# Performance work log

Hardware: AMD Instinct MI355X
Metric: run time of the kernel (lower is better)

The kernel has to match this reference:

```python
import jax, jax.numpy as jnp
import numpy as np

N_NODES = 50000
N_EDGES = 600000
IN_C, HID, OUT_C, HEADS = 128, 64, 16, 4


def setup_inputs() -> dict:
    key = jax.random.key(0)
    ks = jax.random.split(key, 12)
    s = 1.0 / np.sqrt(HID)
    return {
        "x": jax.random.normal(ks[0], (N_NODES, IN_C), dtype=jnp.float32),
        "edge_index": jax.random.randint(ks[1], (2, N_EDGES), 0, N_NODES, dtype=jnp.int64),
        "W_lin": jax.random.normal(ks[2], (IN_C, HID), dtype=jnp.float32) / np.sqrt(IN_C),
        "b_lin": jnp.zeros((HID,), dtype=jnp.float32),
        "Wq": jax.random.normal(ks[3], (HID, HID), dtype=jnp.float32) * s,
        "bq": jnp.zeros((HID,), dtype=jnp.float32),
        "Wk": jax.random.normal(ks[4], (HID, HID), dtype=jnp.float32) * s,
        "bk": jnp.zeros((HID,), dtype=jnp.float32),
        "Wv": jax.random.normal(ks[5], (HID, HID), dtype=jnp.float32) * s,
        "bv": jnp.zeros((HID,), dtype=jnp.float32),
        "W_out": jax.random.normal(ks[6], (HID, OUT_C), dtype=jnp.float32) * s,
        "b_out": jnp.zeros((OUT_C,), dtype=jnp.float32),
    }


def _dna_conv(xs, src, dst, norm, Wq, bq, Wk, bk, Wv, bv):
    # xs: [N, L, C] stacked layer histories. Multi-head attention per edge:
    # query = target node's latest layer, keys/values = source node's full history.
    N, L, C = xs.shape
    d = C // HEADS
    q = (xs[:, -1] @ Wq + bq).reshape(N, HEADS, d)          # [N,H,d]
    k = (xs @ Wk + bk).reshape(N, L, HEADS, d)               # [N,L,H,d]
    v = (xs @ Wv + bv).reshape(N, L, HEADS, d)
    scores = jnp.einsum('ehd,elhd->ehl', q[dst], k[src]) / jnp.sqrt(jnp.float32(d))
    attn = jax.nn.softmax(scores, axis=-1)                   # softmax over layer history
    msg = jnp.einsum('ehl,elhd->ehd', attn, v[src]).reshape(-1, C)  # [E,C]
    msg = msg * norm[:, None]                                # GCN symmetric norm
    return jax.ops.segment_sum(msg, dst, num_segments=N)


def reference(x, edge_index, W_lin, b_lin, Wq, bq, Wk, bk, Wv, bv, W_out, b_out):
    N = x.shape[0]
    loop = jnp.arange(N, dtype=edge_index.dtype)
    src = jnp.concatenate([edge_index[0], loop])
    dst = jnp.concatenate([edge_index[1], loop])
    deg = jax.ops.segment_sum(jnp.ones_like(dst, dtype=x.dtype), dst, num_segments=N)
    dinv = jnp.where(deg > 0, jax.lax.rsqrt(jnp.maximum(deg, 1.0)), 0.0)
    norm = dinv[src] * dinv[dst]

    h = x @ W_lin + b_lin                                    # [N,HID]
    xs = h[:, None, :]
    for _ in range(3):
        out = _dna_conv(xs, src, dst, norm, Wq, bq, Wk, bk, Wv, bv)
        xs = jnp.concatenate([xs, out[:, None, :]], axis=1)
    return xs[:, -1] @ W_out + b_out                          # [N,OUT_C]
```

## Files before the change

### kernel.cpp

```cpp
#include <hip/hip_runtime.h>


__device__ inline unsigned short bf16_rne(float f) {
    unsigned int u = __float_as_uint(f);
    unsigned int r = u + 0x7FFFu + ((u >> 16) & 1u);
    return (unsigned short)(r >> 16);
}
__device__ inline float kf(unsigned int u) { return __uint_as_float(u << 16); }
__device__ inline float vf(unsigned int u) { return __uint_as_float(u & 0xFFFF0000u); }

__global__ __launch_bounds__(256) void hist_dst_k(const int* __restrict__ dst,
                                                  int* __restrict__ cnt, int E) {
    int e = blockIdx.x * 256 + threadIdx.x;
    if (e < E) atomicAdd(&cnt[dst[e]], 1);
}

__global__ __launch_bounds__(256) void scan1_k(const int* __restrict__ cnt,
                                               int* __restrict__ excl,
                                               int* __restrict__ aux,
                                               float* __restrict__ dinv, int N) {
    __shared__ int wtot[4];
    int b = blockIdx.x, t = threadIdx.x;
    int lane = t & 63, w = t >> 6;
    int base = b * 1024 + t * 4;
    int v0 = (base + 0 < N) ? cnt[base + 0] + 1 : 0;
    int v1 = (base + 1 < N) ? cnt[base + 1] + 1 : 0;
    int v2 = (base + 2 < N) ? cnt[base + 2] + 1 : 0;
    int v3 = (base + 3 < N) ? cnt[base + 3] + 1 : 0;
    if (base + 0 < N) dinv[base + 0] = rsqrtf((float)v0);
    if (base + 1 < N) dinv[base + 1] = rsqrtf((float)v1);
    if (base + 2 < N) dinv[base + 2] = rsqrtf((float)v2);
    if (base + 3 < N) dinv[base + 3] = rsqrtf((float)v3);
    int s = v0 + v1 + v2 + v3;
    int incl = s;
#pragma unroll
    for (int off = 1; off < 64; off <<= 1) {
        int u = __shfl_up(incl, off);
        if (lane >= off) incl += u;
    }
    if (lane == 63) wtot[w] = incl;
    __syncthreads();
    int wb = 0;
#pragma unroll
    for (int j = 0; j < 4; ++j) if (j < w) wb += wtot[j];
    int ex = wb + incl - s;
    if (base + 0 < N) excl[base + 0] = ex;
    if (base + 1 < N) excl[base + 1] = ex + v0;
    if (base + 2 < N) excl[base + 2] = ex + v0 + v1;
    if (base + 3 < N) excl[base + 3] = ex + v0 + v1 + v2;
    if (t == 0) aux[b] = wtot[0] + wtot[1] + wtot[2] + wtot[3];
}

__global__ __launch_bounds__(64) void scan_aux_k(int* __restrict__ aux, int nb,
                                                 int* __restrict__ total) {
    int lane = threadIdx.x;
    int v = (lane < nb) ? aux[lane] : 0;
    int incl = v;
#pragma unroll
    for (int off = 1; off < 64; off <<= 1) {
        int u = __shfl_up(incl, off);
        if (lane >= off) incl += u;
    }
    if (lane < nb) aux[lane] = incl - v;
    if (lane == 63) total[0] = incl;
}

__global__ __launch_bounds__(256) void scan_add_k(int* __restrict__ offs,
                                                  const int* __restrict__ aux,
                                                  int* __restrict__ cursor, int N) {
    int i = blockIdx.x * 256 + threadIdx.x;
    if (i < N) {
        int o = offs[i] + aux[i >> 10];
        offs[i] = o;
        cursor[i] = o;
    }
}

__global__ __launch_bounds__(256) void scatter_dst_k(const int* __restrict__ src,
                                                     const int* __restrict__ dst,
                                                     int* __restrict__ cursor,
                                                     int* __restrict__ src_sorted,
                                                     int E, int N) {
    int e = blockIdx.x * 256 + threadIdx.x;
    int M = E + N;
    if (e >= M) return;
    int s, d;
    if (e < E) { s = src[e]; d = dst[e]; }
    else       { s = d = e - E; }
    int pos = atomicAdd(&cursor[d], 1);
    src_sorted[pos] = s;
}

__global__ __launch_bounds__(256) void lin128_64_k(const float* __restrict__ x,
                                                   const float* __restrict__ W,
                                                   const float* __restrict__ b,
                                                   float* __restrict__ y, int N) {
    __shared__ float sW[128 * 64];
    __shared__ float sb[64];
    for (int i = threadIdx.x; i < 128 * 64; i += 256) sW[i] = W[i];
    if (threadIdx.x < 64) sb[threadIdx.x] = b[threadIdx.x];
    __syncthreads();
    int w = threadIdx.x >> 6, c = threadIdx.x & 63;
    int r0 = blockIdx.x * 16 + w * 4;
    if (r0 >= N) return;
    const float* xr[4];
#pragma unroll
    for (int j = 0; j < 4; ++j) {
        int r = r0 + j; if (r > N - 1) r = N - 1;
        xr[j] = x + (size_t)r * 128;
    }
    float acc[4];
#pragma unroll
    for (int j = 0; j < 4; ++j) acc[j] = sb[c];
    for (int k = 0; k < 128; ++k) {
        float wv = sW[k * 64 + c];
#pragma unroll
        for (int j = 0; j < 4; ++j) acc[j] = fmaf(xr[j][k], wv, acc[j]);
    }
#pragma unroll
    for (int j = 0; j < 4; ++j) {
        int r = r0 + j;
        if (r < N) y[(size_t)r * 64 + c] = acc[j];
    }
}

template <bool WRITE_V0>
__global__ __launch_bounds__(192) void proj_qkv_k(const float* __restrict__ X,
                                                  const float* __restrict__ Wq, const float* __restrict__ bq,
                                                  const float* __restrict__ Wk, const float* __restrict__ bk,
                                                  const float* __restrict__ Wv, const float* __restrict__ bv,
                                                  const float* __restrict__ dinv,
                                                  float* __restrict__ q,
                                                  unsigned int* __restrict__ PL,
                                                  unsigned short* __restrict__ V0,
                                                  int N, int l, int RPB) {
    int w = threadIdx.x >> 6;
    int c = threadIdx.x & 63;
    const float* W = (w == 0) ? Wq : (w == 1) ? Wk : Wv;
    const float* B = (w == 0) ? bq : (w == 1) ? bk : bv;
    float wr[64];
#pragma unroll
    for (int k = 0; k < 64; ++k) wr[k] = W[k * 64 + c];
    float bias = B[c];
    int r0 = blockIdx.x * RPB;
    int r1 = r0 + RPB; if (r1 > N) r1 = N;
    unsigned short* PLh = (unsigned short*)PL;
    for (int r = r0; r < r1; ++r) {
        float xv = X[(size_t)r * 64 + c];
        float a = bias;
#pragma unroll
        for (int k = 0; k < 64; ++k) {
            float xk = __int_as_float(__builtin_amdgcn_readlane(__float_as_int(xv), k));
            a = fmaf(xk, wr[k], a);
        }
        if (w == 0) {
            q[(size_t)r * 64 + c] = a * 0.25f;
        } else if (w == 1) {
            PLh[((size_t)r * 192 + l * 64 + c) * 2] = bf16_rne(a);
        } else {
            unsigned short vb = bf16_rne(a * dinv[r]);
            PLh[((size_t)r * 192 + l * 64 + c) * 2 + 1] = vb;
            if (WRITE_V0) V0[(size_t)r * 64 + c] = vb;
        }
    }
}

template <int L>
__global__ __launch_bounds__(256) void attn_g16_k(const int* __restrict__ offs,
                                                  const int* __restrict__ src_sorted,
                                                  const float* __restrict__ dinv,
                                                  const float* __restrict__ q,
                                                  const unsigned int* __restrict__ PL,
                                                  const unsigned short* __restrict__ V0,
                                                  float* __restrict__ out,
                                                  int N) {
    int d  = (blockIdx.x * 256 + threadIdx.x) >> 4;
    int gl = threadIdx.x & 15;
    int gb = threadIdx.x & 48;
    if (d >= N) return;
    int beg = offs[d], end = offs[d + 1];

    float4 qv = make_float4(0.f, 0.f, 0.f, 0.f);
    if (L > 1) qv = *(const float4*)(q + (size_t)d * 64 + gl * 4);

    float a0 = 0.f, a1 = 0.f, a2 = 0.f, a3 = 0.f;

    for (int base = beg; base < end; base += 16) {
        int m = end - base;
        if (m > 16) m = 16;
        int sid = (base + gl < end) ? src_sorted[base + gl] : 0;

        uint4 A0, A1, A2, B0, B1, B2;
        uint2 Av, Bv;
        int s0 = __shfl(sid, gb);
        if (L == 1) {
            Av = *(const uint2*)(V0 + (size_t)s0 * 64 + gl * 4);
        } else {
            const uint4* pp = (const uint4*)(PL + (size_t)s0 * 192) + gl;
            A0 = pp[0];
            A1 = pp[16];
            if (L > 2) A2 = pp[32];
        }

        for (int i = 0; i < m; ++i) {
            int nx = i + 1 < m ? i + 1 : m - 1;
            int sn = __shfl(sid, gb + nx);
            if (L == 1) {
                Bv = *(const uint2*)(V0 + (size_t)sn * 64 + gl * 4);
            } else {
                const uint4* pp = (const uint4*)(PL + (size_t)sn * 192) + gl;
                B0 = pp[0];
                B1 = pp[16];
                if (L > 2) B2 = pp[32];
            }

            if (L == 1) {
                a0 += __uint_as_float((Av.x & 0xFFFFu) << 16);
                a1 += __uint_as_float(Av.x & 0xFFFF0000u);
                a2 += __uint_as_float((Av.y & 0xFFFFu) << 16);
                a3 += __uint_as_float(Av.y & 0xFFFF0000u);
            } else {
                float p0 = qv.x * kf(A0.x);
                p0 = fmaf(qv.y, kf(A0.y), p0);
                p0 = fmaf(qv.z, kf(A0.z), p0);
                p0 = fmaf(qv.w, kf(A0.w), p0);
                float p1 = qv.x * kf(A1.x);
                p1 = fmaf(qv.y, kf(A1.y), p1);
                p1 = fmaf(qv.z, kf(A1.z), p1);
                p1 = fmaf(qv.w, kf(A1.w), p1);
                float p2 = 0.f;
                if (L > 2) {
                    p2 = qv.x * kf(A2.x);
                    p2 = fmaf(qv.y, kf(A2.y), p2);
                    p2 = fmaf(qv.z, kf(A2.z), p2);
                    p2 = fmaf(qv.w, kf(A2.w), p2);
                }
                p0 += __shfl_xor(p0, 1); p0 += __shfl_xor(p0, 2);
                p1 += __shfl_xor(p1, 1); p1 += __shfl_xor(p1, 2);
                if (L > 2) { p2 += __shfl_xor(p2, 1); p2 += __shfl_xor(p2, 2); }
                float w0, w1, w2 = 0.f;
                if (L == 2) {
                    float e = __expf(p1 - p0);
                    w0 = __builtin_amdgcn_rcpf(1.0f + e);
                    w1 = 1.0f - w0;
                } else {
                    float mx = fmaxf(fmaxf(p0, p1), p2);
                    float e0 = __expf(p0 - mx);
                    float e1 = __expf(p1 - mx);
                    float e2 = __expf(p2 - mx);
                    float inv = __builtin_amdgcn_rcpf(e0 + e1 + e2);
                    w0 = e0 * inv; w1 = e1 * inv; w2 = e2 * inv;
                }
                a0 = fmaf(w0, vf(A0.x), a0);
                a1 = fmaf(w0, vf(A0.y), a1);
                a2 = fmaf(w0, vf(A0.z), a2);
                a3 = fmaf(w0, vf(A0.w), a3);
                a0 = fmaf(w1, vf(A1.x), a0);
                a1 = fmaf(w1, vf(A1.y), a1);
                a2 = fmaf(w1, vf(A1.z), a2);
                a3 = fmaf(w1, vf(A1.w), a3);
                if (L > 2) {
                    a0 = fmaf(w2, vf(A2.x), a0);
                    a1 = fmaf(w2, vf(A2.y), a1);
                    a2 = fmaf(w2, vf(A2.z), a2);
                    a3 = fmaf(w2, vf(A2.w), a3);
                }
            }
            if (L == 1) {
                Av = Bv;
            } else {
                A0 = B0; A1 = B1;
                if (L > 2) A2 = B2;
            }
        }
    }
    float dv = dinv[d];
    *(float4*)(out + (size_t)d * 64 + gl * 4) =
        make_float4(a0 * dv, a1 * dv, a2 * dv, a3 * dv);
}

__global__ __launch_bounds__(256) void out_proj_k(const float* __restrict__ xs,
                                                  const float* __restrict__ W,
                                                  const float* __restrict__ b,
                                                  float* __restrict__ y, int N) {
    __shared__ float sW[64 * 16];
    __shared__ float sb[16];
    for (int i = threadIdx.x; i < 64 * 16; i += 256) sW[i] = W[i];
    if (threadIdx.x < 16) sb[threadIdx.x] = b[threadIdx.x];
    __syncthreads();
    int row = blockIdx.x * 16 + (threadIdx.x >> 4);
    int c   = threadIdx.x & 15;
    if (row >= N) return;
    const float* xr = xs + (size_t)row * 64;
    float acc = sb[c];
#pragma unroll 16
    for (int k = 0; k < 64; ++k) acc = fmaf(xr[k], sW[k * 16 + c], acc);
    y[(size_t)row * 16 + c] = acc;
}

extern "C" void kernel_launch(void* const* d_in, const int* in_sizes, int n_in,
                              void* d_out, int out_size, void* d_ws, size_t ws_size,
                              hipStream_t stream) {
    const float* x     = (const float*)d_in[0];
    const int*   ei    = (const int*)d_in[1];
    const float* W_lin = (const float*)d_in[2];
    const float* b_lin = (const float*)d_in[3];
    const float* Wq    = (const float*)d_in[4];
    const float* bq    = (const float*)d_in[5];
    const float* Wk    = (const float*)d_in[6];
    const float* bk    = (const float*)d_in[7];
    const float* Wv    = (const float*)d_in[8];
    const float* bv    = (const float*)d_in[9];
    const float* W_out = (const float*)d_in[10];
    const float* b_out = (const float*)d_in[11];
    float* out = (float*)d_out;

    const int N = in_sizes[0] / 128;
    const int E = in_sizes[1] / 2;
    const int M = E + N;
    const int* srcp = ei;
    const int* dstp = ei + E;

    char* wsb = (char*)d_ws;
    float*          dinv       = (float*)wsb;           wsb += (size_t)N * sizeof(float);
    int*            cnt        = (int*)wsb;             wsb += (size_t)N * sizeof(int);
    int*            offs       = (int*)wsb;             wsb += (size_t)(N + 1) * sizeof(int);
    int*            cursor     = (int*)wsb;             wsb += (size_t)N * sizeof(int);
    int*            aux        = (int*)wsb;             wsb += 64 * sizeof(int);
    int*            src_sorted = (int*)wsb;             wsb += (size_t)M * sizeof(int);
    float*          qb         = (float*)wsb;           wsb += (size_t)N * 64 * sizeof(float);
    unsigned int*   PL         = (unsigned int*)wsb;    wsb += (size_t)N * 192 * sizeof(unsigned int);
    unsigned short* V0p        = (unsigned short*)wsb;  wsb += (size_t)N * 64 * sizeof(unsigned short);
    float*          hA         = (float*)wsb;           wsb += (size_t)N * 64 * sizeof(float);
    float*          outb       = (float*)wsb;

    const int gN   = (N + 255) / 256;
    const int gE   = (E + 255) / 256;
    const int gM   = (M + 255) / 256;
    const int g16  = (N + 15) / 16;
    const int nb   = (N + 1023) / 1024;
    const int RPB  = 16;
    const int gP   = (N + RPB - 1) / RPB;

    hipMemsetAsync(cnt, 0, (size_t)N * sizeof(int), stream);
    hist_dst_k<<<gE, 256, 0, stream>>>(dstp, cnt, E);
    scan1_k<<<nb, 256, 0, stream>>>(cnt, offs, aux, dinv, N);
    scan_aux_k<<<1, 64, 0, stream>>>(aux, nb, offs + N);
    scan_add_k<<<gN, 256, 0, stream>>>(offs, aux, cursor, N);
    scatter_dst_k<<<gM, 256, 0, stream>>>(srcp, dstp, cursor, src_sorted, E, N);

    lin128_64_k<<<g16, 256, 0, stream>>>(x, W_lin, b_lin, hA, N);
    proj_qkv_k<true><<<gP, 192, 0, stream>>>(hA, Wq, bq, Wk, bk, Wv, bv, dinv,
                                             qb, PL, V0p, N, 0, RPB);

    attn_g16_k<1><<<g16, 256, 0, stream>>>(offs, src_sorted, dinv, qb, PL, V0p, outb, N);
    proj_qkv_k<false><<<gP, 192, 0, stream>>>(outb, Wq, bq, Wk, bk, Wv, bv, dinv,
                                              qb, PL, V0p, N, 1, RPB);
    attn_g16_k<2><<<g16, 256, 0, stream>>>(offs, src_sorted, dinv, qb, PL, V0p, outb, N);
    proj_qkv_k<false><<<gP, 192, 0, stream>>>(outb, Wq, bq, Wk, bk, Wv, bv, dinv,
                                              qb, PL, V0p, N, 2, RPB);
    attn_g16_k<3><<<g16, 256, 0, stream>>>(offs, src_sorted, dinv, qb, PL, V0p, outb, N);

    out_proj_k<<<g16, 256, 0, stream>>>(outb, W_out, b_out, out, N);
}
```

Measured before the change: 441.5 us.

## Fuse output projection into final attention, merge scan kernels, deepen prefetch

Folds the aux-block scan into the add kernel: each block reduces the preceding block totals with a wave reduction and also writes the final offset, which removes one launch. The last attention layer now computes the 64-to-16 output projection in-kernel through LDS, so the separate out_proj kernel and its re-read of the hidden features go away. The gather loop also prefetches two neighbours ahead instead of one to hide more memory latency. The cost is extra registers for the deeper prefetch and LDS plus a block barrier in the last layer.

```diff
diff --git a/kernel.cpp b/kernel.cpp
--- a/kernel.cpp
+++ b/kernel.cpp
@@ -51,28 +51,22 @@
     if (t == 0) aux[b] = wtot[0] + wtot[1] + wtot[2] + wtot[3];
 }
 
-__global__ __launch_bounds__(64) void scan_aux_k(int* __restrict__ aux, int nb,
-                                                 int* __restrict__ total) {
-    int lane = threadIdx.x;
-    int v = (lane < nb) ? aux[lane] : 0;
-    int incl = v;
-#pragma unroll
-    for (int off = 1; off < 64; off <<= 1) {
-        int u = __shfl_up(incl, off);
-        if (lane >= off) incl += u;
-    }
-    if (lane < nb) aux[lane] = incl - v;
-    if (lane == 63) total[0] = incl;
-}
-
-__global__ __launch_bounds__(256) void scan_add_k(int* __restrict__ offs,
-                                                  const int* __restrict__ aux,
-                                                  int* __restrict__ cursor, int N) {
+__global__ __launch_bounds__(256) void scan_add2_k(int* __restrict__ offs,
+                                                   const int* __restrict__ aux,
+                                                   const int* __restrict__ cnt,
+                                                   int* __restrict__ cursor,
+                                                   int N, int nb) {
     int i = blockIdx.x * 256 + threadIdx.x;
+    int c = blockIdx.x >> 2;
+    int lane = threadIdx.x & 63;
+    int v = (lane < c && lane < nb) ? aux[lane] : 0;
+#pragma unroll
+    for (int off = 32; off >= 1; off >>= 1) v += __shfl_xor(v, off);
     if (i < N) {
-        int o = offs[i] + aux[i >> 10];
+        int o = offs[i] + v;
         offs[i] = o;
         cursor[i] = o;
+        if (i == N - 1) offs[N] = o + cnt[i] + 1;
     }
 }
 
@@ -165,137 +159,154 @@
     }
 }
 
-template <int L>
+template <int L, bool EMIT_OUT>
 __global__ __launch_bounds__(256) void attn_g16_k(const int* __restrict__ offs,
                                                   const int* __restrict__ src_sorted,
                                                   const float* __restrict__ dinv,
                                                   const float* __restrict__ q,
                                                   const unsigned int* __restrict__ PL,
                                                   const unsigned short* __restrict__ V0,
-                                                  float* __restrict__ out,
+                                                  const float* __restrict__ Wo,
+                                                  const float* __restrict__ bo,
+                                                  float* __restrict__ outv,
                                                   int N) {
+    constexpr int LDSN = EMIT_OUT ? (16 * 68 + 64 * 16 + 16) : 1;
+    __shared__ float lds[LDSN];
+    float* rowS = lds;
+    float* sWo  = lds + 16 * 68;
+    float* sbo  = sWo + 64 * 16;
+    if (EMIT_OUT) {
+        for (int i = threadIdx.x; i < 64 * 16; i += 256) sWo[i] = Wo[i];
+        if (threadIdx.x < 16) sbo[threadIdx.x] = bo[threadIdx.x];
+    }
+
     int d  = (blockIdx.x * 256 + threadIdx.x) >> 4;
     int gl = threadIdx.x & 15;
     int gb = threadIdx.x & 48;
-    if (d >= N) return;
-    int beg = offs[d], end = offs[d + 1];
-
-    float4 qv = make_float4(0.f, 0.f, 0.f, 0.f);
-    if (L > 1) qv = *(const float4*)(q + (size_t)d * 64 + gl * 4);
-
     float a0 = 0.f, a1 = 0.f, a2 = 0.f, a3 = 0.f;
-
-    for (int base = beg; base < end; base += 16) {
-        int m = end - base;
-        if (m > 16) m = 16;
-        int sid = (base + gl < end) ? src_sorted[base + gl] : 0;
-
-        uint4 A0, A1, A2, B0, B1, B2;
-        uint2 Av, Bv;
-        int s0 = __shfl(sid, gb);
-        if (L == 1) {
-            Av = *(const uint2*)(V0 + (size_t)s0 * 64 + gl * 4);
-        } else {
-            const uint4* pp = (const uint4*)(PL + (size_t)s0 * 192) + gl;
-            A0 = pp[0];
-            A1 = pp[16];
-            if (L > 2) A2 = pp[32];
-        }
-
-        for (int i = 0; i < m; ++i) {
-            int nx = i + 1 < m ? i + 1 : m - 1;
-            int sn = __shfl(sid, gb + nx);
+    float dv = 0.f;
+
+    if (d < N) {
+        dv = dinv[d];
+        int beg = offs[d], end = offs[d + 1];
+        float4 qv = make_float4(0.f, 0.f, 0.f, 0.f);
+        if (L > 1) qv = *(const float4*)(q + (size_t)d * 64 + gl * 4);
+
+        for (int base = beg; base < end; base += 16) {
+            int m = end - base;
+            if (m > 16) m = 16;
+            int sid = (base + gl < end) ? src_sorted[base + gl] : 0;
+            int mm1 = m - 1;
+#define SIDAT(j) __shfl(sid, gb + ((j) < mm1 ? (j) : mm1))
+            uint4 A0, A1, A2, B0, B1, B2, C0, C1, C2;
+            uint2 Av, Bv, Cv;
+            int sA = SIDAT(0), sB = SIDAT(1);
             if (L == 1) {
-                Bv = *(const uint2*)(V0 + (size_t)sn * 64 + gl * 4);
+                Av = *(const uint2*)(V0 + (size_t)sA * 64 + gl * 4);
+                Bv = *(const uint2*)(V0 + (size_t)sB * 64 + gl * 4);
             } else {
-                const uint4* pp = (const uint4*)(PL + (size_t)sn * 192) + gl;
-                B0 = pp[0];
-                B1 = pp[16];
-                if (L > 2) B2 = pp[32];
+                const uint4* pa = (const uint4*)(PL + (size_t)sA * 192) + gl;
+                A0 = pa[0]; A1 = pa[16]; if (L > 2) A2 = pa[32];
+                const uint4* pb = (const uint4*)(PL + (size_t)sB * 192) + gl;
+                B0 = pb[0]; B1 = pb[16]; if (L > 2) B2 = pb[32];
             }
 
-            if (L == 1) {
-                a0 += __uint_as_float((Av.x & 0xFFFFu) << 16);
-                a1 += __uint_as_float(Av.x & 0xFFFF0000u);
-                a2 += __uint_as_float((Av.y & 0xFFFFu) << 16);
-                a3 += __uint_as_float(Av.y & 0xFFFF0000u);
-            } else {
-                float p0 = qv.x * kf(A0.x);
-                p0 = fmaf(qv.y, kf(A0.y), p0);
-                p0 = fmaf(qv.z, kf(A0.z), p0);
-                p0 = fmaf(qv.w, kf(A0.w), p0);
-                float p1 = qv.x * kf(A1.x);
-                p1 = fmaf(qv.y, kf(A1.y), p1);
-                p1 = fmaf(qv.z, kf(A1.z), p1);
-                p1 = fmaf(qv.w, kf(A1.w), p1);
-                float p2 = 0.f;
-                if (L > 2) {
-                    p2 = qv.x * kf(A2.x);
-                    p2 = fmaf(qv.y, kf(A2.y), p2);
-                    p2 = fmaf(qv.z, kf(A2.z), p2);
-                    p2 = fmaf(qv.w, kf(A2.w), p2);
+            for (int i = 0; i < m; ++i) {
+                int sC = SIDAT(i + 2);
+                if (L == 1) {
+                    Cv = *(const uint2*)(V0 + (size_t)sC * 64 + gl * 4);
+                } else {
+                    const uint4* pc = (const uint4*)(PL + (size_t)sC * 192) + gl;
+                    C0 = pc[0]; C1 = pc[16]; if (L > 2) C2 = pc[32];
                 }
-                p0 += __shfl_xor(p0, 1); p0 += __shfl_xor(p0, 2);
-                p1 += __shfl_xor(p1, 1); p1 += __shfl_xor(p1, 2);
-                if (L > 2) { p2 += __shfl_xor(p2, 1); p2 += __shfl_xor(p2, 2); }
-                float w0, w1, w2 = 0.f;
-                if (L == 2) {
-                    float e = __expf(p1 - p0);
-                    w0 = __builtin_amdgcn_rcpf(1.0f + e);
-                    w1 = 1.0f - w0;
+
+                if (L == 1) {
+                    a0 += __uint_as_float((Av.x & 0xFFFFu) << 16);
+                    a1 += __uint_as_float(Av.x & 0xFFFF0000u);
+                    a2 += __uint_as_float((Av.y & 0xFFFFu) << 16);
+                    a3 += __uint_as_float(Av.y & 0xFFFF0000u);
                 } else {
-                    float mx = fmaxf(fmaxf(p0, p1), p2);
-                    float e0 = __expf(p0 - mx);
-                    float e1 = __expf(p1 - mx);
-                    float e2 = __expf(p2 - mx);
-                    float inv = __builtin_amdgcn_rcpf(e0 + e1 + e2);
-                    w0 = e0 * inv; w1 = e1 * inv; w2 = e2 * inv;
+                    float p0 = qv.x * kf(A0.x);
+                    p0 = fmaf(qv.y, kf(A0.y), p0);
+                    p0 = fmaf(qv.z, kf(A0.z), p0);
+                    p0 = fmaf(qv.w, kf(A0.w), p0);
+                    float p1 = qv.x * kf(A1.x);
+                    p1 = fmaf(qv.y, kf(A1.y), p1);
+                    p1 = fmaf(qv.z, kf(A1.z), p1);
+                    p1 = fmaf(qv.w, kf(A1.w), p1);
+                    float p2 = 0.f;
+                    if (L > 2) {
+                        p2 = qv.x * kf(A2.x);
+                        p2 = fmaf(qv.y, kf(A2.y), p2);
+                        p2 = fmaf(qv.z, kf(A2.z), p2);
+                        p2 = fmaf(qv.w, kf(A2.w), p2);
+                    }
+                    p0 += __shfl_xor(p0, 1); p0 += __shfl_xor(p0, 2);
+                    p1 += __shfl_xor(p1, 1); p1 += __shfl_xor(p1, 2);
+                    if (L > 2) { p2 += __shfl_xor(p2, 1); p2 += __shfl_xor(p2, 2); }
+                    float w0, w1, w2 = 0.f;
+                    if (L == 2) {
+                        float e = __expf(p1 - p0);
+                        w0 = __builtin_amdgcn_rcpf(1.0f + e);
+                        w1 = 1.0f - w0;
+                    } else {
+                        float mx = fmaxf(fmaxf(p0, p1), p2);
+                        float e0 = __expf(p0 - mx);
+                        float e1 = __expf(p1 - mx);
+                        float e2 = __expf(p2 - mx);
+                        float inv = __builtin_amdgcn_rcpf(e0 + e1 + e2);
+                        w0 = e0 * inv; w1 = e1 * inv; w2 = e2 * inv;
+                    }
+                    a0 = fmaf(w0, vf(A0.x), a0);
+                    a1 = fmaf(w0, vf(A0.y), a1);
+                    a2 = fmaf(w0, vf(A0.z), a2);
+                    a3 = fmaf(w0, vf(A0.w), a3);
+                    a0 = fmaf(w1, vf(A1.x), a0);
+                    a1 = fmaf(w1, vf(A1.y), a1);
+                    a2 = fmaf(w1, vf(A1.z), a2);
+                    a3 = fmaf(w1, vf(A1.w), a3);
+                    if (L > 2) {
+                        a0 = fmaf(w2, vf(A2.x), a0);
+                        a1 = fmaf(w2, vf(A2.y), a1);
+                        a2 = fmaf(w2, vf(A2.z), a2);
+                        a3 = fmaf(w2, vf(A2.w), a3);
+                    }
                 }
-                a0 = fmaf(w0, vf(A0.x), a0);
-                a1 = fmaf(w0, vf(A0.y), a1);
-                a2 = fmaf(w0, vf(A0.z), a2);
-                a3 = fmaf(w0, vf(A0.w), a3);
-                a0 = fmaf(w1, vf(A1.x), a0);
-                a1 = fmaf(w1, vf(A1.y), a1);
-                a2 = fmaf(w1, vf(A1.z), a2);
-                a3 = fmaf(w1, vf(A1.w), a3);
-                if (L > 2) {
-                    a0 = fmaf(w2, vf(A2.x), a0);
-                    a1 = fmaf(w2, vf(A2.y), a1);
-                    a2 = fmaf(w2, vf(A2.z), a2);
-                    a3 = fmaf(w2, vf(A2.w), a3);
+                if (L == 1) {
+                    Av = Bv; Bv = Cv;
+                } else {
+                    A0 = B0; A1 = B1; B0 = C0; B1 = C1;
+                    if (L > 2) { A2 = B2; B2 = C2; }
                 }
             }
-            if (L == 1) {
-                Av = Bv;
-            } else {
-                A0 = B0; A1 = B1;
-                if (L > 2) A2 = B2;
-            }
-        }
-    }
-    float dv = dinv[d];
-    *(float4*)(out + (size_t)d * 64 + gl * 4) =
-        make_float4(a0 * dv, a1 * dv, a2 * dv, a3 * dv);
-}
-
-__global__ __launch_bounds__(256) void out_proj_k(const float* __restrict__ xs,
-                                                  const float* __restrict__ W,
-                                                  const float* __restrict__ b,
-                                                  float* __restrict__ y, int N) {
-    __shared__ float sW[64 * 16];
-    __shared__ float sb[16];
-    for (int i = threadIdx.x; i < 64 * 16; i += 256) sW[i] = W[i];
-    if (threadIdx.x < 16) sb[threadIdx.x] = b[threadIdx.x];
-    __syncthreads();
-    int row = blockIdx.x * 16 + (threadIdx.x >> 4);
-    int c   = threadIdx.x & 15;
-    if (row >= N) return;
-    const float* xr = xs + (size_t)row * 64;
-    float acc = sb[c];
+#undef SIDAT
+        }
+    }
+
+    if (EMIT_OUT) {
+        int w16 = threadIdx.x >> 4;
+        if (d < N) {
+            rowS[w16 * 68 + gl * 4 + 0] = a0 * dv;
+            rowS[w16 * 68 + gl * 4 + 1] = a1 * dv;
+            rowS[w16 * 68 + gl * 4 + 2] = a2 * dv;
+            rowS[w16 * 68 + gl * 4 + 3] = a3 * dv;
+        }
+        __syncthreads();
+        int node = threadIdx.x >> 4;
+        int co   = threadIdx.x & 15;
+        int dn   = blockIdx.x * 16 + node;
+        if (dn < N) {
+            float acc = sbo[co];
 #pragma unroll 16
-    for (int k = 0; k < 64; ++k) acc = fmaf(xr[k], sW[k * 16 + c], acc);
-    y[(size_t)row * 16 + c] = acc;
+            for (int k = 0; k < 64; ++k)
+                acc = fmaf(rowS[node * 68 + k], sWo[k * 16 + co], acc);
+            outv[(size_t)dn * 16 + co] = acc;
+        }
+    } else {
+        if (d < N)
+            *(float4*)(outv + (size_t)d * 64 + gl * 4) =
+                make_float4(a0 * dv, a1 * dv, a2 * dv, a3 * dv);
+    }
 }
 
 extern "C" void kernel_launch(void* const* d_in, const int* in_sizes, int n_in,
@@ -345,21 +356,21 @@
     hipMemsetAsync(cnt, 0, (size_t)N * sizeof(int), stream);
     hist_dst_k<<<gE, 256, 0, stream>>>(dstp, cnt, E);
     scan1_k<<<nb, 256, 0, stream>>>(cnt, offs, aux, dinv, N);
-    scan_aux_k<<<1, 64, 0, stream>>>(aux, nb, offs + N);
-    scan_add_k<<<gN, 256, 0, stream>>>(offs, aux, cursor, N);
+    scan_add2_k<<<gN, 256, 0, stream>>>(offs, aux, cnt, cursor, N, nb);
     scatter_dst_k<<<gM, 256, 0, stream>>>(srcp, dstp, cursor, src_sorted, E, N);
 
     lin128_64_k<<<g16, 256, 0, stream>>>(x, W_lin, b_lin, hA, N);
     proj_qkv_k<true><<<gP, 192, 0, stream>>>(hA, Wq, bq, Wk, bk, Wv, bv, dinv,
                                              qb, PL, V0p, N, 0, RPB);
 
-    attn_g16_k<1><<<g16, 256, 0, stream>>>(offs, src_sorted, dinv, qb, PL, V0p, outb, N);
+    attn_g16_k<1, false><<<g16, 256, 0, stream>>>(offs, src_sorted, dinv, qb, PL, V0p,
+                                                  nullptr, nullptr, outb, N);
     proj_qkv_k<false><<<gP, 192, 0, stream>>>(outb, Wq, bq, Wk, bk, Wv, bv, dinv,
                                               qb, PL, V0p, N, 1, RPB);
-    attn_g16_k<2><<<g16, 256, 0, stream>>>(offs, src_sorted, dinv, qb, PL, V0p, outb, N);
+    attn_g16_k<2, false><<<g16, 256, 0, stream>>>(offs, src_sorted, dinv, qb, PL, V0p,
+                                                  nullptr, nullptr, outb, N);
     proj_qkv_k<false><<<gP, 192, 0, stream>>>(outb, Wq, bq, Wk, bk, Wv, bv, dinv,
                                               qb, PL, V0p, N, 2, RPB);
-    attn_g16_k<3><<<g16, 256, 0, stream>>>(offs, src_sorted, dinv, qb, PL, V0p, outb, N);
-
-    out_proj_k<<<g16, 256, 0, stream>>>(outb, W_out, b_out, out, N);
-}
+    attn_g16_k<3, true><<<g16, 256, 0, stream>>>(offs, src_sorted, dinv, qb, PL, V0p,
+                                                 W_out, b_out, out, N);
+}
```

New measurement: 430.9 us. 2.4% less time.
